# Optimization experiments

Hardware: AMD Instinct MI355X
Metric: run time of the kernel (lower is better)

The kernel has to match this reference:

```python
import jax, jax.numpy as jnp
import numpy as np

B, S, D = 2, 2048, 2048
H = 16
NOPE, ROPE, DV = 128, 64, 128
DQK = NOPE + ROPE  # 192
QLR, KVLR = 1536, 512


def setup_inputs() -> dict:
    key = jax.random.key(0)
    ks = jax.random.split(key, 8)
    hidden_states = jax.random.normal(ks[0], (B, S, D), dtype=jnp.float32) * 0.02
    sequence_mask = jnp.ones((B, S), dtype=bool)
    # rotary frequencies (complex exponential split into cos/sin), theta=10000
    inv_freq = 1.0 / (10000.0 ** (np.arange(0, ROPE, 2, dtype=np.float32) / ROPE))
    angles = np.outer(np.arange(S, dtype=np.float32), inv_freq)  # [S, ROPE//2]
    freqs_cos = jnp.asarray(np.cos(angles), dtype=jnp.float32)
    freqs_sin = jnp.asarray(np.sin(angles), dtype=jnp.float32)
    def lin(k, fan_in, fan_out):
        return jax.random.normal(k, (fan_in, fan_out), dtype=jnp.float32) / np.sqrt(fan_in)
    return {
        'hidden_states': hidden_states,
        'sequence_mask': sequence_mask,
        'freqs_cos': freqs_cos,
        'freqs_sin': freqs_sin,
        'Wq_down': lin(ks[1], D, QLR),
        'Wkv_down': lin(ks[2], D, KVLR + ROPE),
        'Wq_up': lin(ks[3], QLR, H * DQK),
        'Wkv_up': lin(ks[4], KVLR, H * (DV + NOPE)),
        'Wo': lin(ks[5], H * DV, D),
    }


def _rmsnorm(x, eps=1e-5):
    return x * jax.lax.rsqrt(jnp.mean(x * x, axis=-1, keepdims=True) + eps)


def _apply_rope(x, cos, sin):
    # x: [B,S,H,d] with interleaved (real, imag) pairs; cos/sin: [S, d//2]
    b, s, h, d = x.shape
    xr = x.reshape(b, s, h, d // 2, 2)
    x0, x1 = xr[..., 0], xr[..., 1]
    c = cos[None, :s, None, :]
    sn = sin[None, :s, None, :]
    y = jnp.stack([x0 * c - x1 * sn, x0 * sn + x1 * c], axis=-1)
    return y.reshape(b, s, h, d)


def reference(hidden_states, sequence_mask, freqs_cos, freqs_sin,
              Wq_down, Wkv_down, Wq_up, Wkv_up, Wo):
    b, s, _ = hidden_states.shape
    # Q path: down-project -> rmsnorm -> up-project
    q_latent = _rmsnorm(hidden_states @ Wq_down)
    q = (q_latent @ Wq_up).reshape(b, s, H, DQK)
    q_nope, q_rope = q[..., :NOPE], q[..., NOPE:]
    q_rope = _apply_rope(q_rope, freqs_cos, freqs_sin)
    q = jnp.concatenate([q_rope, q_nope], axis=-1)  # [B,S,H,DQK]
    # KV path
    kvdr = hidden_states @ Wkv_down  # [B,S,KVLR+ROPE]
    kv_latent, k_rope = kvdr[..., :KVLR], kvdr[..., KVLR:]
    k_rope = _apply_rope(k_rope.reshape(b, s, 1, ROPE), freqs_cos, freqs_sin)
    k_rope = jnp.broadcast_to(k_rope, (b, s, H, ROPE))
    kv = _rmsnorm(kv_latent) @ Wkv_up  # [B,S,H*(NOPE+DV)]
    k_nope = kv[..., :H * NOPE].reshape(b, s, H, NOPE)
    v = kv[..., H * NOPE:].reshape(b, s, H, DV)
    k = jnp.concatenate([k_rope, k_nope], axis=-1)  # [B,S,H,DQK]
    # causal attention (flash_attn_varlen with full masks == per-batch causal)
    scale = 1.0 / np.sqrt(DQK)
    scores = jnp.einsum('bqhd,bkhd->bhqk', q, k) * scale
    causal = jnp.tril(jnp.ones((s, s), dtype=bool))
    mask = causal[None, None, :, :] & sequence_mask[:, None, None, :]
    scores = jnp.where(mask, scores, jnp.float32(-1e9))
    attn = jax.nn.softmax(scores, axis=-1)
    out = jnp.einsum('bhqk,bkhd->bqhd', attn, v).reshape(b, s, H * DV)
    return out @ Wo
```

## Files before the change

kernel.cpp:

```cpp
#include <hip/hip_runtime.h>
#include <math.h>


typedef unsigned short u16;
typedef __attribute__((ext_vector_type(8))) __bf16 bf16x8;
typedef __attribute__((ext_vector_type(4))) float f32x4;

#define DEV static __device__ __forceinline__

#if __has_builtin(__builtin_amdgcn_exp2f)
#define EXP2(x) __builtin_amdgcn_exp2f(x)
#else
#define EXP2(x) exp2f(x)
#endif

DEV float b2f(u16 v) { return __uint_as_float(((unsigned int)v) << 16); }
DEV u16 f2b(float f) {
  unsigned int u = __float_as_uint(f);
  u += 0x7fffu + ((u >> 16) & 1u);
  return (u16)(u >> 16);
}
DEV u16 f2b_hw(float f) {
  __bf16 h = (__bf16)f;
  u16 r;
  __builtin_memcpy(&r, &h, 2);
  return r;
}

DEV float waveReduceSum(float v) {
  #pragma unroll
  for (int o = 32; o > 0; o >>= 1) v += __shfl_down(v, o, 64);
  return v;
}

DEV void gld16(const u16* g, u16* l) {
  __builtin_amdgcn_global_load_lds((const __attribute__((address_space(1))) void*)g,
                                   (__attribute__((address_space(3))) void*)l, 16, 0, 0);
}

__global__ __launch_bounds__(256)
void cvt_f32_bf16(const float* __restrict__ in, u16* __restrict__ out, int n4) {
  int i = blockIdx.x * 256 + threadIdx.x;
  if (i < n4) {
    float4 v = reinterpret_cast<const float4*>(in)[i];
    ushort4 o;
    o.x = f2b(v.x); o.y = f2b(v.y); o.z = f2b(v.z); o.w = f2b(v.w);
    reinterpret_cast<ushort4*>(out)[i] = o;
  }
}

__global__ __launch_bounds__(256)
void transpose_all(const float* __restrict__ Wqd, const float* __restrict__ Wkvd,
                   const float* __restrict__ Wqu, const float* __restrict__ Wkvu,
                   const float* __restrict__ Wo,
                   u16* __restrict__ W13T, u16* __restrict__ WquT,
                   u16* __restrict__ WkvuT, u16* __restrict__ WoT) {
  __shared__ u16 tile[32][33];
  int n = blockIdx.x;
  const float* in; u16* out; int R, C, gx, local;
  if (n < 3072)       { in = Wqd;  out = W13T;                        R = 2048; C = 1536; gx = 48;  local = n; }
  else if (n < 4224)  { in = Wkvd; out = W13T + (size_t)1536 * 2048;  R = 2048; C = 576;  gx = 18;  local = n - 3072; }
  else if (n < 8832)  { in = Wqu;  out = WquT;                        R = 1536; C = 3072; gx = 96;  local = n - 4224; }
  else if (n < 10880) { in = Wkvu; out = WkvuT;                       R = 512;  C = 4096; gx = 128; local = n - 8832; }
  else                { in = Wo;   out = WoT;                         R = 2048; C = 2048; gx = 64;  local = n - 10880; }
  int c0 = (local % gx) * 32, r0 = (local / gx) * 32;
  for (int i = threadIdx.y; i < 32; i += 8)
    tile[i][threadIdx.x] = f2b(in[(size_t)(r0 + i) * C + c0 + threadIdx.x]);
  __syncthreads();
  for (int i = threadIdx.y; i < 32; i += 8)
    out[(size_t)(c0 + i) * R + r0 + threadIdx.x] = tile[threadIdx.x][i];
}

template<int OUT_BF16>
DEV void gemm_body(const u16* __restrict__ A, const u16* __restrict__ BT, void* __restrict__ Cp,
                   int N, int K, int gx, int nwg, int orig, u16* As, u16* Bs) {
  const int tid = threadIdx.x;
  const int lane = tid & 63;
  const int wave = tid >> 6;
  const int wm = (wave >> 1) * 64;
  const int wn = (wave & 1) * 64;
  const int q = lane >> 4;
  const int l16 = lane & 15;

  const int cpx = nwg >> 3;
  const int swz = (orig & 7) * cpx + (orig >> 3);
  const int bm = (swz / gx) * 128;
  const int bn = (swz % gx) * 128;

  f32x4 zero = {0.f, 0.f, 0.f, 0.f};
  f32x4 acc[4][4];
  #pragma unroll
  for (int i = 0; i < 4; i++)
    #pragma unroll
    for (int j = 0; j < 4; j++) acc[i][j] = zero;

  for (int k0 = 0; k0 < K; k0 += 32) {
    #pragma unroll
    for (int i = 0; i < 2; i++) {
      int jb = i * 256 + wave * 64;
      int u = jb + lane;
      int row = u >> 2;
      int kq = (u & 3) ^ ((u >> 3) & 3);
      gld16(A + (size_t)(bm + row) * K + k0 + kq * 8, As + jb * 8);
      int rB = bn + row;
      if (rB >= N) rB = N - 1;
      gld16(BT + (size_t)rB * K + k0 + kq * 8, Bs + jb * 8);
    }
    __syncthreads();
    bf16x8 af[4], bfr[4];
    #pragma unroll
    for (int t = 0; t < 4; t++) {
      int rowA = wm + t * 16 + l16;
      int rowB = wn + t * 16 + l16;
      int uA = (rowA << 2) | (q ^ ((rowA >> 1) & 3));
      int uB = (rowB << 2) | (q ^ ((rowB >> 1) & 3));
      af[t]  = *reinterpret_cast<const bf16x8*>(As + uA * 8);
      bfr[t] = *reinterpret_cast<const bf16x8*>(Bs + uB * 8);
    }
    #pragma unroll
    for (int mt = 0; mt < 4; mt++)
      #pragma unroll
      for (int nt = 0; nt < 4; nt++)
        acc[mt][nt] = __builtin_amdgcn_mfma_f32_16x16x32_bf16(af[mt], bfr[nt], acc[mt][nt], 0, 0, 0);
    __syncthreads();
  }

  float* Cf = (float*)Cp;
  u16* Cb = (u16*)Cp;
  #pragma unroll
  for (int mt = 0; mt < 4; mt++) {
    #pragma unroll
    for (int nt = 0; nt < 4; nt++) {
      int col = bn + wn + nt * 16 + l16;
      if (col < N) {
        int row0 = bm + wm + mt * 16 + q * 4;
        #pragma unroll
        for (int r = 0; r < 4; r++) {
          size_t idx = (size_t)(row0 + r) * N + col;
          float v = acc[mt][nt][r];
          if (OUT_BF16) Cb[idx] = f2b(v); else Cf[idx] = v;
        }
      }
    }
  }
}

template<int OUT_BF16>
__global__ __launch_bounds__(256)
void gemm_bt(const u16* __restrict__ A, const u16* __restrict__ BT, void* __restrict__ Cp,
             int N, int K) {
  __shared__ __attribute__((aligned(16))) u16 As[4096];
  __shared__ __attribute__((aligned(16))) u16 Bs[4096];
  const int gx = gridDim.x;
  const int nwg = gx * gridDim.y;
  const int orig = blockIdx.y * gx + blockIdx.x;
  gemm_body<OUT_BF16>(A, BT, Cp, N, K, gx, nwg, orig, As, Bs);
}

__global__ __launch_bounds__(256)
void gemm_up2(const u16* __restrict__ qlat, const u16* __restrict__ WquT, u16* __restrict__ q2,
              const u16* __restrict__ kvl, const u16* __restrict__ WkvuT, u16* __restrict__ kvb) {
  __shared__ __attribute__((aligned(16))) u16 As[4096];
  __shared__ __attribute__((aligned(16))) u16 Bs[4096];
  int n = blockIdx.x;
  if (n < 768) gemm_body<1>(qlat, WquT, q2, 3072, 1536, 24, 768, n, As, Bs);
  else         gemm_body<1>(kvl, WkvuT, kvb, 4096, 512, 32, 1024, n - 768, As, Bs);
}

__global__ __launch_bounds__(256)
void norm_split(const float* __restrict__ t13, const float* __restrict__ fc, const float* __restrict__ fs,
                u16* __restrict__ qlat, u16* __restrict__ kvl, u16* __restrict__ krope) {
  __shared__ float red[4];
  __shared__ float s_scale;
  int lane = threadIdx.x & 63, wid = threadIdx.x >> 6;
  if (blockIdx.x < 4096) {
    int row = blockIdx.x;
    const float* x = t13 + (size_t)row * 2112;
    float ss = 0.f;
    for (int i = threadIdx.x; i < 1536; i += 256) { float v = x[i]; ss += v * v; }
    ss = waveReduceSum(ss);
    if (lane == 0) red[wid] = ss;
    __syncthreads();
    if (threadIdx.x == 0)
      s_scale = rsqrtf((red[0] + red[1] + red[2] + red[3]) * (1.0f / 1536.0f) + 1e-5f);
    __syncthreads();
    float sc = s_scale;
    u16* o = qlat + (size_t)row * 1536;
    for (int i = threadIdx.x; i < 1536; i += 256) o[i] = f2b(x[i] * sc);
  } else {
    int row = blockIdx.x - 4096;
    int s = row & 2047;
    const float* x = t13 + (size_t)row * 2112 + 1536;
    float ss = 0.f;
    for (int i = threadIdx.x; i < 512; i += 256) { float v = x[i]; ss += v * v; }
    ss = waveReduceSum(ss);
    if (lane == 0) red[wid] = ss;
    __syncthreads();
    if (threadIdx.x == 0)
      s_scale = rsqrtf((red[0] + red[1] + red[2] + red[3]) * (1.0f / 512.0f) + 1e-5f);
    __syncthreads();
    float sc = s_scale;
    for (int i = threadIdx.x; i < 512; i += 256) kvl[(size_t)row * 512 + i] = f2b(x[i] * sc);
    if (threadIdx.x < 32) {
      int i = threadIdx.x;
      float cc = fc[s * 32 + i], sn = fs[s * 32 + i];
      float x0 = x[512 + 2 * i], x1 = x[512 + 2 * i + 1];
      krope[(size_t)row * 64 + 2 * i]     = f2b(x0 * cc - x1 * sn);
      krope[(size_t)row * 64 + 2 * i + 1] = f2b(x0 * sn + x1 * cc);
    }
  }
}

__global__ __launch_bounds__(256)
void rope_pack_q(const u16* __restrict__ q2, const float* __restrict__ fc, const float* __restrict__ fs,
                 u16* __restrict__ Q) {
  const float scale = 0.10411756711f;
  int bs = blockIdx.x;
  int b = bs >> 11, s = bs & 2047;
  __shared__ float c[32], sn[32];
  if (threadIdx.x < 32) {
    c[threadIdx.x] = fc[s * 32 + threadIdx.x];
    sn[threadIdx.x] = fs[s * 32 + threadIdx.x];
  }
  __syncthreads();
  const u16* qrow = q2 + (size_t)bs * 3072;
  for (int t = threadIdx.x; t < 512; t += 256) {
    int h = t >> 5, i = t & 31;
    float x0 = b2f(qrow[h * 192 + 128 + 2 * i]);
    float x1 = b2f(qrow[h * 192 + 128 + 2 * i + 1]);
    size_t base = ((size_t)(b * 16 + h) * 2048 + s) * 192;
    Q[base + 2 * i]     = f2b((x0 * c[i] - x1 * sn[i]) * scale);
    Q[base + 2 * i + 1] = f2b((x0 * sn[i] + x1 * c[i]) * scale);
  }
  for (int t = threadIdx.x; t < 2048; t += 256) {
    int h = t >> 7, j = t & 127;
    Q[((size_t)(b * 16 + h) * 2048 + s) * 192 + 64 + j] = f2b(b2f(qrow[h * 192 + j]) * scale);
  }
}

__global__ __launch_bounds__(256)
void assemble_kv2(const u16* __restrict__ kvb, const u16* __restrict__ krope,
                  u16* __restrict__ Kc, u16* __restrict__ Vt) {
  int ks = blockIdx.x;
  int bh = blockIdx.y;
  int b = bh >> 4, h = bh & 15;
  int t = threadIdx.x;
  if (t < 192) {
    int kq = t >> 3, sl = t & 7;
    int s = ks * 8 + sl;
    size_t bs = (size_t)(b * 2048 + s);
    uint4 v;
    if (kq < 8) v = *reinterpret_cast<const uint4*>(krope + bs * 64 + kq * 8);
    else        v = *reinterpret_cast<const uint4*>(kvb + bs * 4096 + h * 128 + (kq - 8) * 8);
    *reinterpret_cast<uint4*>(Kc + (((size_t)bh * 24 + kq) * 2048 + s) * 8) = v;
  }
  if (t < 128) {
    int dv = t;
    u16 tmp[8];
    #pragma unroll
    for (int j = 0; j < 8; j++) {
      int s = ks * 8 + j;
      tmp[j] = kvb[(size_t)(b * 2048 + s) * 4096 + 2048 + h * 128 + dv];
    }
    *reinterpret_cast<uint4*>(Vt + (((size_t)bh * 256 + ks) * 128 + dv) * 8) = *reinterpret_cast<uint4*>(tmp);
  }
}

__global__ __launch_bounds__(256, 2)
void flash_attn8(const u16* __restrict__ Q, const u16* __restrict__ Kc,
                 const u16* __restrict__ Vt, u16* __restrict__ O) {
  __shared__ __attribute__((aligned(16))) u16 Ks[2][24 * 64 * 8];
  __shared__ __attribute__((aligned(16))) u16 Vs[8 * 128 * 8];
  __shared__ __attribute__((aligned(16))) u16 Ps[4 * 16 * 72];

  const int blk = blockIdx.x;
  const int bh = ((blk & 7) << 2) | (blk >> 7);
  const int tpair = (blk >> 3) & 15;
  const int b = bh >> 4, h = bh & 15;
  const int tid = threadIdx.x, lane = tid & 63, wave = tid >> 6;
  const int quad = lane >> 4, l16 = lane & 15;
  u16* PsW = Ps + wave * 16 * 72;

  bf16x8 onesf;
  #pragma unroll
  for (int j = 0; j < 8; j++) onesf[j] = (l16 == 0) ? (__bf16)1.0f : (__bf16)0.0f;

  auto stageK = [&](u16* KsB, int kk) {
    #pragma unroll
    for (int ii = 0; ii < 6; ii++) {
      int kq = wave * 6 + ii;
      gld16(Kc + (((size_t)bh * 24 + kq) * 2048 + kk + lane) * 8, KsB + kq * 64 * 8);
    }
  };
  auto stageV = [&](int kk) {
    #pragma unroll
    for (int jj = 0; jj < 4; jj++) {
      int vc = wave * 4 + jj, kc = vc >> 1, dvh = vc & 1;
      gld16(Vt + (((size_t)bh * 256 + (kk >> 3) + kc) * 128 + dvh * 64 + lane) * 8,
            Vs + (kc * 128 + dvh * 64) * 8);
    }
  };

  for (int phase = 0; phase < 2; phase++) {
    const int qt = phase == 0 ? tpair : 31 - tpair;
    const int q0 = qt * 64;
    const int nk = (qt + 1) * 64;

    bf16x8 qf[6];
    {
      int qrow = q0 + wave * 16 + l16;
      const u16* qp = Q + ((size_t)bh * 2048 + qrow) * 192 + quad * 8;
      #pragma unroll
      for (int kc = 0; kc < 6; kc++)
        qf[kc] = *reinterpret_cast<const bf16x8*>(qp + kc * 32);
    }

    f32x4 zero = {0.f, 0.f, 0.f, 0.f};
    f32x4 oacc[9];
    #pragma unroll
    for (int nt = 0; nt < 9; nt++) oacc[nt] = zero;

    for (int k0 = 0; k0 < nk; k0 += 64) {
      const int cur = (k0 >> 6) & 1;
      const bool hasnext = (k0 + 64 < nk);

      __builtin_amdgcn_s_barrier();
      __builtin_amdgcn_sched_barrier(0);
      if (k0 == 0) stageK(Ks[0], 0);
      stageV(k0);
      if (hasnext) {
        stageK(Ks[cur ^ 1], k0 + 64);
        asm volatile("s_waitcnt vmcnt(10)" ::: "memory");
      } else {
        asm volatile("s_waitcnt vmcnt(4)" ::: "memory");
      }
      __builtin_amdgcn_sched_barrier(0);
      __builtin_amdgcn_s_barrier();
      __builtin_amdgcn_sched_barrier(0);

      const u16* KsC = Ks[cur];

      f32x4 sacc[4];
      #pragma unroll
      for (int nt = 0; nt < 4; nt++) sacc[nt] = zero;
      #pragma unroll
      for (int kc = 0; kc < 6; kc++) {
        #pragma unroll
        for (int nt = 0; nt < 4; nt++) {
          bf16x8 kb = *reinterpret_cast<const bf16x8*>(KsC + ((kc * 4 + quad) * 64 + nt * 16 + l16) * 8);
          sacc[nt] = __builtin_amdgcn_mfma_f32_16x16x32_bf16(qf[kc], kb, sacc[nt], 0, 0, 0);
        }
      }

      if (k0 + 63 <= q0 + wave * 16) {
        #pragma unroll
        for (int r = 0; r < 4; r++) {
          #pragma unroll
          for (int nt = 0; nt < 4; nt++) {
            float p = EXP2(sacc[nt][r]);
            PsW[(quad * 4 + r) * 72 + nt * 16 + l16] = f2b_hw(p);
          }
        }
      } else {
        #pragma unroll
        for (int r = 0; r < 4; r++) {
          int qrow_g = q0 + wave * 16 + quad * 4 + r;
          #pragma unroll
          for (int nt = 0; nt < 4; nt++) {
            int key = k0 + nt * 16 + l16;
            float e = EXP2(sacc[nt][r]);
            float p = (key <= qrow_g) ? e : 0.f;
            PsW[(quad * 4 + r) * 72 + nt * 16 + l16] = f2b_hw(p);
          }
        }
      }

      if (hasnext) asm volatile("s_waitcnt vmcnt(6)" ::: "memory");
      else         asm volatile("s_waitcnt vmcnt(0)" ::: "memory");
      __builtin_amdgcn_sched_barrier(0);
      __builtin_amdgcn_s_barrier();
      __builtin_amdgcn_sched_barrier(0);

      #pragma unroll
      for (int kcp = 0; kcp < 2; kcp++) {
        bf16x8 pa = *reinterpret_cast<const bf16x8*>(PsW + l16 * 72 + kcp * 32 + quad * 8);
        #pragma unroll
        for (int nt = 0; nt < 8; nt++) {
          bf16x8 vb = *reinterpret_cast<const bf16x8*>(Vs + ((kcp * 4 + quad) * 128 + nt * 16 + l16) * 8);
          oacc[nt] = __builtin_amdgcn_mfma_f32_16x16x32_bf16(pa, vb, oacc[nt], 0, 0, 0);
        }
        oacc[8] = __builtin_amdgcn_mfma_f32_16x16x32_bf16(pa, onesf, oacc[8], 0, 0, 0);
      }
    }

    #pragma unroll
    for (int r = 0; r < 4; r++) {
      float l = __shfl(oacc[8][r], lane & 48, 64);
      float inv = 1.0f / l;
      int s = q0 + wave * 16 + quad * 4 + r;
      #pragma unroll
      for (int nt = 0; nt < 8; nt++)
        O[((size_t)b * 2048 + s) * 2048 + h * 128 + nt * 16 + l16] = f2b(oacc[nt][r] * inv);
    }
  }
}

extern "C" void kernel_launch(void* const* d_in, const int* in_sizes, int n_in,
                              void* d_out, int out_size, void* d_ws, size_t ws_size,
                              hipStream_t stream) {
  (void)in_sizes; (void)n_in; (void)out_size; (void)ws_size;
  const float* hs   = (const float*)d_in[0];
  const float* fc   = (const float*)d_in[2];
  const float* fs   = (const float*)d_in[3];
  const float* Wqd  = (const float*)d_in[4];
  const float* Wkvd = (const float*)d_in[5];
  const float* Wqu  = (const float*)d_in[6];
  const float* Wkvu = (const float*)d_in[7];
  const float* Wo   = (const float*)d_in[8];

  char* ws = (char*)d_ws;
  size_t off = 0;
  auto alloc = [&](size_t bytes) { size_t o = off; off += (bytes + 255) & ~(size_t)255; return o; };
  const size_t oHS   = alloc(16777216);
  const size_t oRA   = alloc(16777216);
  const size_t oRB   = alloc(25165824);
  const size_t oRC   = alloc(12582912);
  const size_t oRD   = alloc(25165824);
  const size_t oRE   = alloc(34603008);
  const size_t oKVL  = alloc(4194304);
  const size_t oKR   = alloc(524288);
  const size_t oW13T  = alloc(8650752);
  const size_t oWquT  = alloc(9437184);
  const size_t oWkvuT = alloc(4194304);
  const size_t oWoT   = alloc(8388608);

  u16* hs_bf = (u16*)(ws + oHS);
  u16* Vt   = (u16*)(ws + oRA);
  u16* q2   = (u16*)(ws + oRB);
  u16* Kc   = (u16*)(ws + oRB);
  u16* qlat = (u16*)(ws + oRC);
  u16* Qb   = (u16*)(ws + oRD);
  float* t13 = (float*)(ws + oRE);
  u16* kvb  = (u16*)(ws + oRE);
  u16* attn_out = (u16*)(ws + oRE);
  u16* kvl  = (u16*)(ws + oKVL);
  u16* krope = (u16*)(ws + oKR);
  u16* W13T  = (u16*)(ws + oW13T);
  u16* WquT  = (u16*)(ws + oWquT);
  u16* WkvuT = (u16*)(ws + oWkvuT);
  u16* WoT   = (u16*)(ws + oWoT);

  cvt_f32_bf16<<<8192, 256, 0, stream>>>(hs, hs_bf, 2097152);
  transpose_all<<<14976, dim3(32, 8), 0, stream>>>(Wqd, Wkvd, Wqu, Wkvu, Wo, W13T, WquT, WkvuT, WoT);

  gemm_bt<0><<<dim3(17, 32), 256, 0, stream>>>(hs_bf, W13T, t13, 2112, 2048);
  norm_split<<<8192, 256, 0, stream>>>(t13, fc, fs, qlat, kvl, krope);
  gemm_up2<<<1792, 256, 0, stream>>>(qlat, WquT, q2, kvl, WkvuT, kvb);
  rope_pack_q<<<4096, 256, 0, stream>>>(q2, fc, fs, Qb);
  assemble_kv2<<<dim3(256, 32), 256, 0, stream>>>(kvb, krope, Kc, Vt);
  flash_attn8<<<dim3(512), 256, 0, stream>>>(Qb, Kc, Vt, attn_out);
  gemm_bt<0><<<dim3(16, 32), 256, 0, stream>>>(attn_out, WoT, (float*)d_out, 2048, 2048);
}
```

Baseline: 446.2 us.

## Use 256x256 GEMM tiles with triple-buffered async LDS pipeline

Replaces the 128x128 single-buffered GEMM body with a 256x256 tile per 512-thread workgroup, each wave computing a 128x64 subtile. Global-to-LDS loads now run through a three-stage ring with vmcnt waits and one barrier per k-step, and prefetch is interleaved with the MFMA bursts under raised priority. The aim is to cut global traffic per flop and hide load latency. The cost is fewer workgroups (e.g. 144 and 128 for the down and output projections) on a 256-CU device, so occupancy and tail effects may hurt, plus higher register and LDS use.

```diff
diff --git a/kernel.cpp b/kernel.cpp
--- a/kernel.cpp
+++ b/kernel.cpp
@@ -72,72 +72,116 @@
 }
 
 template<int OUT_BF16>
-DEV void gemm_body(const u16* __restrict__ A, const u16* __restrict__ BT, void* __restrict__ Cp,
-                   int N, int K, int gx, int nwg, int orig, u16* As, u16* Bs) {
+DEV void gemm256_body(const u16* __restrict__ A, const u16* __restrict__ BT, void* __restrict__ Cp,
+                      int N, int K, int gx, int nwg, int orig,
+                      u16 (*As)[8192], u16 (*Bs)[8192]) {
   const int tid = threadIdx.x;
   const int lane = tid & 63;
   const int wave = tid >> 6;
-  const int wm = (wave >> 1) * 64;
-  const int wn = (wave & 1) * 64;
+  const int wm = (wave >> 2) * 128;
+  const int wn = (wave & 3) * 64;
   const int q = lane >> 4;
   const int l16 = lane & 15;
 
   const int cpx = nwg >> 3;
   const int swz = (orig & 7) * cpx + (orig >> 3);
-  const int bm = (swz / gx) * 128;
-  const int bn = (swz % gx) * 128;
-
-  f32x4 zero = {0.f, 0.f, 0.f, 0.f};
-  f32x4 acc[4][4];
-  #pragma unroll
-  for (int i = 0; i < 4; i++)
-    #pragma unroll
-    for (int j = 0; j < 4; j++) acc[i][j] = zero;
-
-  for (int k0 = 0; k0 < K; k0 += 32) {
+  const int bm = (swz / gx) * 256;
+  const int bn = (swz % gx) * 256;
+
+  auto stageA = [&](int buf, int k0) {
     #pragma unroll
     for (int i = 0; i < 2; i++) {
-      int jb = i * 256 + wave * 64;
-      int u = jb + lane;
+      int ub = i * 512 + wave * 64;
+      int u = ub + lane;
       int row = u >> 2;
       int kq = (u & 3) ^ ((u >> 3) & 3);
-      gld16(A + (size_t)(bm + row) * K + k0 + kq * 8, As + jb * 8);
+      gld16(A + (size_t)(bm + row) * K + k0 + kq * 8, As[buf] + ub * 8);
+    }
+  };
+  auto stageB = [&](int buf, int k0) {
+    #pragma unroll
+    for (int i = 0; i < 2; i++) {
+      int ub = i * 512 + wave * 64;
+      int u = ub + lane;
+      int row = u >> 2;
+      int kq = (u & 3) ^ ((u >> 3) & 3);
       int rB = bn + row;
       if (rB >= N) rB = N - 1;
-      gld16(BT + (size_t)rB * K + k0 + kq * 8, Bs + jb * 8);
-    }
-    __syncthreads();
-    bf16x8 af[4], bfr[4];
-    #pragma unroll
-    for (int t = 0; t < 4; t++) {
-      int rowA = wm + t * 16 + l16;
-      int rowB = wn + t * 16 + l16;
-      int uA = (rowA << 2) | (q ^ ((rowA >> 1) & 3));
-      int uB = (rowB << 2) | (q ^ ((rowB >> 1) & 3));
-      af[t]  = *reinterpret_cast<const bf16x8*>(As + uA * 8);
-      bfr[t] = *reinterpret_cast<const bf16x8*>(Bs + uB * 8);
-    }
+      gld16(BT + (size_t)rB * K + k0 + kq * 8, Bs[buf] + ub * 8);
+    }
+  };
+
+  f32x4 zero = {0.f, 0.f, 0.f, 0.f};
+  f32x4 acc[8][4];
+  #pragma unroll
+  for (int i = 0; i < 8; i++)
+    #pragma unroll
+    for (int j = 0; j < 4; j++) acc[i][j] = zero;
+
+  const int nt = K >> 5;
+  stageA(0, 0);  stageB(0, 0);
+  stageA(1, 32); stageB(1, 32);
+
+  for (int t = 0; t < nt; ++t) {
+    const int cur = t % 3;
+    if (t + 1 < nt) asm volatile("s_waitcnt vmcnt(4)" ::: "memory");
+    else            asm volatile("s_waitcnt vmcnt(0)" ::: "memory");
+    __builtin_amdgcn_sched_barrier(0);
+    __builtin_amdgcn_s_barrier();
+    __builtin_amdgcn_sched_barrier(0);
+
+    const u16* Ab = As[cur];
+    const u16* Bb = Bs[cur];
+    const int nxt = (t + 2) % 3;
+    const bool pre = (t + 2) < nt;
+    const int kpre = (t + 2) * 32;
+
+    bf16x8 bfr[4], af[4];
+    #pragma unroll
+    for (int j = 0; j < 4; j++) {
+      int rowB = wn + j * 16 + l16;
+      bfr[j] = *reinterpret_cast<const bf16x8*>(Bb + (((rowB) << 2) | (q ^ ((rowB >> 1) & 3))) * 8);
+      int rowA = wm + j * 16 + l16;
+      af[j] = *reinterpret_cast<const bf16x8*>(Ab + (((rowA) << 2) | (q ^ ((rowA >> 1) & 3))) * 8);
+    }
+    if (pre) stageA(nxt, kpre);
+    __builtin_amdgcn_s_setprio(1);
     #pragma unroll
     for (int mt = 0; mt < 4; mt++)
       #pragma unroll
-      for (int nt = 0; nt < 4; nt++)
-        acc[mt][nt] = __builtin_amdgcn_mfma_f32_16x16x32_bf16(af[mt], bfr[nt], acc[mt][nt], 0, 0, 0);
-    __syncthreads();
+      for (int j = 0; j < 4; j++)
+        acc[mt][j] = __builtin_amdgcn_mfma_f32_16x16x32_bf16(af[mt], bfr[j], acc[mt][j], 0, 0, 0);
+    __builtin_amdgcn_s_setprio(0);
+
+    bf16x8 af2[4];
+    #pragma unroll
+    for (int j = 0; j < 4; j++) {
+      int rowA = wm + (j + 4) * 16 + l16;
+      af2[j] = *reinterpret_cast<const bf16x8*>(Ab + (((rowA) << 2) | (q ^ ((rowA >> 1) & 3))) * 8);
+    }
+    if (pre) stageB(nxt, kpre);
+    __builtin_amdgcn_s_setprio(1);
+    #pragma unroll
+    for (int mt = 0; mt < 4; mt++)
+      #pragma unroll
+      for (int j = 0; j < 4; j++)
+        acc[mt + 4][j] = __builtin_amdgcn_mfma_f32_16x16x32_bf16(af2[mt], bfr[j], acc[mt + 4][j], 0, 0, 0);
+    __builtin_amdgcn_s_setprio(0);
   }
 
   float* Cf = (float*)Cp;
   u16* Cb = (u16*)Cp;
   #pragma unroll
-  for (int mt = 0; mt < 4; mt++) {
-    #pragma unroll
-    for (int nt = 0; nt < 4; nt++) {
-      int col = bn + wn + nt * 16 + l16;
+  for (int mt = 0; mt < 8; mt++) {
+    #pragma unroll
+    for (int j = 0; j < 4; j++) {
+      int col = bn + wn + j * 16 + l16;
       if (col < N) {
         int row0 = bm + wm + mt * 16 + q * 4;
         #pragma unroll
         for (int r = 0; r < 4; r++) {
           size_t idx = (size_t)(row0 + r) * N + col;
-          float v = acc[mt][nt][r];
+          float v = acc[mt][j][r];
           if (OUT_BF16) Cb[idx] = f2b(v); else Cf[idx] = v;
         }
       }
@@ -146,25 +190,25 @@
 }
 
 template<int OUT_BF16>
-__global__ __launch_bounds__(256)
-void gemm_bt(const u16* __restrict__ A, const u16* __restrict__ BT, void* __restrict__ Cp,
+__global__ __launch_bounds__(512, 1)
+void gemm256(const u16* __restrict__ A, const u16* __restrict__ BT, void* __restrict__ Cp,
              int N, int K) {
-  __shared__ __attribute__((aligned(16))) u16 As[4096];
-  __shared__ __attribute__((aligned(16))) u16 Bs[4096];
+  __shared__ __attribute__((aligned(16))) u16 As[3][8192];
+  __shared__ __attribute__((aligned(16))) u16 Bs[3][8192];
   const int gx = gridDim.x;
   const int nwg = gx * gridDim.y;
   const int orig = blockIdx.y * gx + blockIdx.x;
-  gemm_body<OUT_BF16>(A, BT, Cp, N, K, gx, nwg, orig, As, Bs);
-}
-
-__global__ __launch_bounds__(256)
+  gemm256_body<OUT_BF16>(A, BT, Cp, N, K, gx, nwg, orig, As, Bs);
+}
+
+__global__ __launch_bounds__(512, 1)
 void gemm_up2(const u16* __restrict__ qlat, const u16* __restrict__ WquT, u16* __restrict__ q2,
               const u16* __restrict__ kvl, const u16* __restrict__ WkvuT, u16* __restrict__ kvb) {
-  __shared__ __attribute__((aligned(16))) u16 As[4096];
-  __shared__ __attribute__((aligned(16))) u16 Bs[4096];
+  __shared__ __attribute__((aligned(16))) u16 As[3][8192];
+  __shared__ __attribute__((aligned(16))) u16 Bs[3][8192];
   int n = blockIdx.x;
-  if (n < 768) gemm_body<1>(qlat, WquT, q2, 3072, 1536, 24, 768, n, As, Bs);
-  else         gemm_body<1>(kvl, WkvuT, kvb, 4096, 512, 32, 1024, n - 768, As, Bs);
+  if (n < 192) gemm256_body<1>(qlat, WquT, q2, 3072, 1536, 12, 192, n, As, Bs);
+  else         gemm256_body<1>(kvl, WkvuT, kvb, 4096, 512, 16, 256, n - 192, As, Bs);
 }
 
 __global__ __launch_bounds__(256)
@@ -453,11 +497,11 @@
   cvt_f32_bf16<<<8192, 256, 0, stream>>>(hs, hs_bf, 2097152);
   transpose_all<<<14976, dim3(32, 8), 0, stream>>>(Wqd, Wkvd, Wqu, Wkvu, Wo, W13T, WquT, WkvuT, WoT);
 
-  gemm_bt<0><<<dim3(17, 32), 256, 0, stream>>>(hs_bf, W13T, t13, 2112, 2048);
+  gemm256<0><<<dim3(9, 16), 512, 0, stream>>>(hs_bf, W13T, t13, 2112, 2048);
   norm_split<<<8192, 256, 0, stream>>>(t13, fc, fs, qlat, kvl, krope);
-  gemm_up2<<<1792, 256, 0, stream>>>(qlat, WquT, q2, kvl, WkvuT, kvb);
+  gemm_up2<<<448, 512, 0, stream>>>(qlat, WquT, q2, kvl, WkvuT, kvb);
   rope_pack_q<<<4096, 256, 0, stream>>>(q2, fc, fs, Qb);
   assemble_kv2<<<dim3(256, 32), 256, 0, stream>>>(kvb, krope, Kc, Vt);
   flash_attn8<<<dim3(512), 256, 0, stream>>>(Qb, Kc, Vt, attn_out);
-  gemm_bt<0><<<dim3(16, 32), 256, 0, stream>>>(attn_out, WoT, (float*)d_out, 2048, 2048);
-}
+  gemm256<0><<<dim3(8, 16), 512, 0, stream>>>(attn_out, WoT, (float*)d_out, 2048, 2048);
+}
```

New measurement: 442.1 us. Within noise of the previous version (-0.9%).
